# Kernel optimization log

Hardware: AMD Instinct MI355X
Metric: run time of the kernel (lower is better)

## Reference

```python
import jax, jax.numpy as jnp
import numpy as np

INPUT_SIZE = 24
OUTPUT_SIZE = 24
HIDDEN = 40
BATCH = 4096
SEQ = 256


def setup_inputs() -> dict:
    key = jax.random.key(0)
    ks = jax.random.split(key, 7)
    s = 1.0 / np.sqrt(HIDDEN)  # torch RNN/Linear default uniform bound
    x = jax.random.normal(ks[0], (BATCH, SEQ, INPUT_SIZE), dtype=jnp.float32)
    W_ih = jax.random.uniform(ks[1], (3 * HIDDEN, INPUT_SIZE), jnp.float32, -s, s)
    W_hh = jax.random.uniform(ks[2], (3 * HIDDEN, HIDDEN), jnp.float32, -s, s)
    b_ih = jax.random.uniform(ks[3], (3 * HIDDEN,), jnp.float32, -s, s)
    b_hh = jax.random.uniform(ks[4], (3 * HIDDEN,), jnp.float32, -s, s)
    W_fc = jax.random.uniform(ks[5], (OUTPUT_SIZE, HIDDEN), jnp.float32, -s, s)
    b_fc = jax.random.uniform(ks[6], (OUTPUT_SIZE,), jnp.float32, -s, s)
    return {"x": x, "W_ih": W_ih, "W_hh": W_hh, "b_ih": b_ih,
            "b_hh": b_hh, "W_fc": W_fc, "b_fc": b_fc}


def _gru_forward(x, W_ih, W_hh, b_ih, b_hh):
    # PyTorch GRU gate order: reset, update, new. Precompute input projections.
    B, T, _ = x.shape
    H = W_hh.shape[1]
    xg = jnp.einsum('bti,gi->btg', x, W_ih) + b_ih  # [B, T, 3H]

    def step(h, xg_t):
        hg = h @ W_hh.T + b_hh                      # [B, 3H]
        xr, xz, xn = jnp.split(xg_t, 3, axis=-1)
        hr, hz, hn = jnp.split(hg, 3, axis=-1)
        r = jax.nn.sigmoid(xr + hr)
        z = jax.nn.sigmoid(xz + hz)
        n = jnp.tanh(xn + r * hn)
        h_new = (1.0 - z) * n + z * h
        return h_new, h_new

    h0 = jnp.zeros((B, H), dtype=x.dtype)
    hT, outs = jax.lax.scan(step, h0, jnp.swapaxes(xg, 0, 1))  # outs: [T, B, H]
    return jnp.swapaxes(outs, 0, 1), hT                        # [B, T, H], [B, H]


def reference(x, W_ih, W_hh, b_ih, b_hh, W_fc, b_fc):
    seq_out, hT = _gru_forward(x, W_ih, W_hh, b_ih, b_hh)
    H = W_hh.shape[1]
    out = seq_out.reshape(-1, H)                   # [B*T, H]
    out = jax.nn.sigmoid(out @ W_fc.T + b_fc)      # [B*T, output_size]
    hidden = hT[None]                              # [n_layers=1, B, H]
    return out, hidden
```

## Files before the change

### kernel.cpp

```cpp
#include <hip/hip_runtime.h>
#include <math.h>

typedef __attribute__((ext_vector_type(8))) short short8;
typedef __attribute__((ext_vector_type(4))) float f32x4;

namespace {
constexpr int BATCH = 4096;
constexpr int SEQT  = 256;
constexpr int INSZ  = 24;
constexpr int H     = 40;
constexpr int NOUT  = 24;
constexpr int R     = 16;
constexpr int NT    = 256;

__device__ __forceinline__ unsigned short f2bf(float f) {
  unsigned int u = __float_as_uint(f);
  return (unsigned short)((u + 0x7FFFu + ((u >> 16) & 1u)) >> 16);
}
__device__ __forceinline__ unsigned short cvt_bf16(float f) {
  float r;
  asm("v_cvt_pk_bf16_f32 %0, %1, %2" : "=v"(r) : "v"(f), "v"(f));
  return (unsigned short)__float_as_uint(r);
}
__device__ __forceinline__ unsigned int cvt_pk2(float lo, float hi) {
  float r;
  asm("v_cvt_pk_bf16_f32 %0, %1, %2" : "=v"(r) : "v"(lo), "v"(hi));
  return __float_as_uint(r);
}
__device__ __forceinline__ float4 ld4(const float* p) {
  return *reinterpret_cast<const float4*>(p);
}
__device__ __forceinline__ float sigm(float v) {
  return __builtin_amdgcn_rcpf(1.0f + __builtin_amdgcn_exp2f(v * -1.442695041f));
}
__device__ __forceinline__ float tanh_fast(float v) {
  return fmaf(2.0f,
              __builtin_amdgcn_rcpf(1.0f + __builtin_amdgcn_exp2f(v * -2.885390082f)),
              -1.0f);
}
}

#define BAR()                                              \
  asm volatile("s_waitcnt lgkmcnt(0)" ::: "memory");       \
  __builtin_amdgcn_s_barrier();                            \
  __builtin_amdgcn_sched_barrier(0);

#define MFMA16(A, Bf, C) __builtin_amdgcn_mfma_f32_16x16x32_bf16((A), (Bf), (C), 0, 0, 0)

__global__ __launch_bounds__(NT) void gru_ilp2(
    const float* __restrict__ x, const float* __restrict__ Wih,
    const float* __restrict__ Whh, const float* __restrict__ bih,
    const float* __restrict__ bhh, const float* __restrict__ Wfc,
    const float* __restrict__ bfc, float* __restrict__ out,
    float* __restrict__ hid) {
  __shared__ __align__(16) unsigned short Abuf[4 * 1024];

  const int tid = threadIdx.x;
  const int l   = tid & 63;
  const int w   = tid >> 6;
  const int lm  = l & 15;
  const int lq  = l >> 4;
  const int gb0 = blockIdx.x * R;

  reinterpret_cast<uint4*>(Abuf)[tid]       = make_uint4(0, 0, 0, 0);
  reinterpret_cast<uint4*>(Abuf)[tid + 256] = make_uint4(0, 0, 0, 0);

  const int aBase0 = ((lm * 64 + lq * 8)      ^ ((lm & 7) << 3));
  const int aBase1 = ((lm * 64 + lq * 8 + 32) ^ ((lm & 7) << 3));

  short8 B[4][2];
  float bias[4] = {0, 0, 0, 0};
  float hold[2][2] = {{0, 0}, {0, 0}};
  int aw[2] = {0, 0};
  int u = 0;
  bool gvalid = false;
  if (w < 3) {
    u = w * 16 + lm;
    gvalid = (u < H);
#pragma unroll
    for (int z = 0; z < 4; ++z) {
#pragma unroll
      for (int kt = 0; kt < 2; ++kt) {
        short8 b;
#pragma unroll
        for (int j = 0; j < 8; ++j) {
          const int k = kt * 32 + lq * 8 + j;
          float v = 0.0f;
          if (gvalid) {
            if (z == 0)      v = (k < 24) ? Wih[u * 24 + k]          : Whh[u * 40 + (k - 24)];
            else if (z == 1) v = (k < 24) ? Wih[(40 + u) * 24 + k]   : Whh[(40 + u) * 40 + (k - 24)];
            else if (z == 2) v = (k < 24) ? Wih[(80 + u) * 24 + k]   : 0.0f;
            else             v = (k < 24) ? 0.0f                     : Whh[(80 + u) * 40 + (k - 24)];
          }
          b[j] = (short)f2bf(v);
        }
        B[z][kt] = b;
      }
    }
    if (gvalid) {
      bias[0] = bih[u] + bhh[u];
      bias[1] = bih[40 + u] + bhh[40 + u];
      bias[2] = bih[80 + u];
      bias[3] = bhh[80 + u];
    }
#pragma unroll
    for (int i = 0; i < 2; ++i) {
      const int arow = lq * 4 + i;
      aw[i] = ((arow * 64 + 24 + u) ^ ((arow & 7) << 3));
    }
  }

  short8 F[2][2];
  float biasF[2] = {0, 0};
  float* orow[2][2] = {{nullptr, nullptr}, {nullptr, nullptr}};
  const float* xpg[2] = {nullptr, nullptr};
  int xw0 = 0;
  bool xv = false;
  float4 aQ1 = make_float4(0,0,0,0), aQ2 = make_float4(0,0,0,0);
  float4 aQ3 = make_float4(0,0,0,0), aQ0 = make_float4(0,0,0,0);
  float4 bQ1 = make_float4(0,0,0,0), bQ2 = make_float4(0,0,0,0);
  float4 bQ3 = make_float4(0,0,0,0), bQ0 = make_float4(0,0,0,0);
  if (w == 3) {
#pragma unroll
    for (int f = 0; f < 2; ++f) {
      const int o = f * 16 + lm;
#pragma unroll
      for (int kt = 0; kt < 2; ++kt) {
        short8 b;
#pragma unroll
        for (int j = 0; j < 8; ++j) {
          const int k = kt * 32 + lq * 8 + j;
          const float v = (o < NOUT && k >= 24) ? Wfc[o * H + (k - 24)] : 0.0f;
          b[j] = (short)f2bf(v);
        }
        F[f][kt] = b;
      }
      biasF[f] = (o < NOUT) ? bfc[o] : 0.0f;
    }
#pragma unroll
    for (int g = 0; g < 2; ++g)
#pragma unroll
      for (int i = 0; i < 2; ++i)
        orow[g][i] = out + ((size_t)(gb0 + g * 8 + lq * 2 + i) * SEQT) * NOUT;

    xv = (l < 48);
    const int xr = l / 6, xc = (l - xr * 6) * 4;
    const int ar_ = ((xr >> 1) << 2) + (xr & 1);
    if (xv) {
      xpg[0] = x + ((size_t)(gb0 + xr) * SEQT) * INSZ + xc;
      xpg[1] = x + ((size_t)(gb0 + 8 + xr) * SEQT) * INSZ + xc;
    }
    xw0 = ((ar_ * 64 + xc) ^ ((ar_ & 7) << 3));
  }

  const f32x4 kZero = {0.0f, 0.0f, 0.0f, 0.0f};

  __syncthreads();

  if (w == 3 && xv) {
    const float4 v0 = ld4(xpg[0]);
    *reinterpret_cast<uint2*>(&Abuf[xw0]) =
        make_uint2(cvt_pk2(v0.x, v0.y), cvt_pk2(v0.z, v0.w));
    const float4 v1 = ld4(xpg[1]);
    *reinterpret_cast<uint2*>(&Abuf[2048 + xw0]) =
        make_uint2(cvt_pk2(v1.x, v1.y), cvt_pk2(v1.z, v1.w));
    aQ1 = ld4(xpg[0] + 1 * INSZ);  bQ1 = ld4(xpg[1] + 1 * INSZ);
    aQ2 = ld4(xpg[0] + 2 * INSZ);  bQ2 = ld4(xpg[1] + 2 * INSZ);
    aQ3 = ld4(xpg[0] + 3 * INSZ);  bQ3 = ld4(xpg[1] + 3 * INSZ);
    aQ0 = ld4(xpg[0] + 4 * INSZ);  bQ0 = ld4(xpg[1] + 4 * INSZ);
  }
  __syncthreads();

#define GATE2(BO, NBO)                                                          \
  if (w < 3) {                                                                  \
    const short8 A00 = *reinterpret_cast<const short8*>(&Abuf[(BO) + aBase0]);  \
    const short8 A01 = *reinterpret_cast<const short8*>(&Abuf[(BO) + aBase1]);  \
    const short8 A10 = *reinterpret_cast<const short8*>(&Abuf[2048 + (BO) + aBase0]); \
    const short8 A11 = *reinterpret_cast<const short8*>(&Abuf[2048 + (BO) + aBase1]); \
    f32x4 ar0 = MFMA16(A00, B[0][0], kZero);                                    \
    f32x4 az0 = MFMA16(A00, B[1][0], kZero);                                    \
    f32x4 ax0 = MFMA16(A00, B[2][0], kZero);                                    \
    f32x4 ah0 = MFMA16(A00, B[3][0], kZero);                                    \
    f32x4 ar1 = MFMA16(A10, B[0][0], kZero);                                    \
    f32x4 az1 = MFMA16(A10, B[1][0], kZero);                                    \
    f32x4 ax1 = MFMA16(A10, B[2][0], kZero);                                    \
    f32x4 ah1 = MFMA16(A10, B[3][0], kZero);                                    \
    ar0 = MFMA16(A01, B[0][1], ar0);                                            \
    az0 = MFMA16(A01, B[1][1], az0);                                            \
    ah0 = MFMA16(A01, B[3][1], ah0);                                            \
    ar1 = MFMA16(A11, B[0][1], ar1);                                            \
    az1 = MFMA16(A11, B[1][1], az1);                                            \
    ah1 = MFMA16(A11, B[3][1], ah1);                                            \
    _Pragma("unroll")                                                           \
    for (int i = 0; i < 2; ++i) {                                               \
      const float rr = sigm(ar0[i] + bias[0]);                                  \
      const float zz = sigm(az0[i] + bias[1]);                                  \
      const float nn = tanh_fast(fmaf(rr, ah0[i] + bias[3], ax0[i] + bias[2])); \
      const float h  = fmaf(zz, hold[0][i] - nn, nn);                           \
      hold[0][i] = h;                                                           \
      if (gvalid) Abuf[(NBO) + aw[i]] = cvt_bf16(h);                            \
    }                                                                           \
    _Pragma("unroll")                                                           \
    for (int i = 0; i < 2; ++i) {                                               \
      const float rr = sigm(ar1[i] + bias[0]);                                  \
      const float zz = sigm(az1[i] + bias[1]);                                  \
      const float nn = tanh_fast(fmaf(rr, ah1[i] + bias[3], ax1[i] + bias[2])); \
      const float h  = fmaf(zz, hold[1][i] - nn, nn);                           \
      hold[1][i] = h;                                                           \
      if (gvalid) Abuf[2048 + (NBO) + aw[i]] = cvt_bf16(h);                     \
    }                                                                           \
  }

#define XSTAGE2(T, TBO, XSa, XSb)                                               \
  if (xv) {                                                                     \
    if ((T) < SEQT) {                                                           \
      *reinterpret_cast<uint2*>(&Abuf[(TBO) + xw0]) =                           \
          make_uint2(cvt_pk2(XSa.x, XSa.y), cvt_pk2(XSa.z, XSa.w));             \
      *reinterpret_cast<uint2*>(&Abuf[2048 + (TBO) + xw0]) =                    \
          make_uint2(cvt_pk2(XSb.x, XSb.y), cvt_pk2(XSb.z, XSb.w));             \
    }                                                                           \
    if ((T) + 4 < SEQT) {                                                       \
      XSa = ld4(xpg[0] + (size_t)((T) + 4) * INSZ);                             \
      XSb = ld4(xpg[1] + (size_t)((T) + 4) * INSZ);                             \
    }                                                                           \
  }

#define FC2(T, BO)                                                              \
  {                                                                             \
    const short8 hA00 = *reinterpret_cast<const short8*>(&Abuf[(BO) + aBase0]); \
    const short8 hA01 = *reinterpret_cast<const short8*>(&Abuf[(BO) + aBase1]); \
    const short8 hA10 = *reinterpret_cast<const short8*>(&Abuf[2048 + (BO) + aBase0]); \
    const short8 hA11 = *reinterpret_cast<const short8*>(&Abuf[2048 + (BO) + aBase1]); \
    f32x4 f00 = MFMA16(hA00, F[0][0], kZero);                                   \
    f32x4 f01 = MFMA16(hA00, F[1][0], kZero);                                   \
    f32x4 f10 = MFMA16(hA10, F[0][0], kZero);                                   \
    f32x4 f11 = MFMA16(hA10, F[1][0], kZero);                                   \
    f00 = MFMA16(hA01, F[0][1], f00);                                           \
    f01 = MFMA16(hA01, F[1][1], f01);                                           \
    f10 = MFMA16(hA11, F[0][1], f10);                                           \
    f11 = MFMA16(hA11, F[1][1], f11);                                           \
    _Pragma("unroll")                                                           \
    for (int i = 0; i < 2; ++i) {                                               \
      orow[0][i][(size_t)(T) * NOUT + lm] = sigm(f00[i] + biasF[0]);            \
      orow[1][i][(size_t)(T) * NOUT + lm] = sigm(f10[i] + biasF[0]);            \
      if (lm < 8) {                                                             \
        orow[0][i][(size_t)(T) * NOUT + 16 + lm] = sigm(f01[i] + biasF[1]);     \
        orow[1][i][(size_t)(T) * NOUT + 16 + lm] = sigm(f11[i] + biasF[1]);     \
      }                                                                         \
    }                                                                           \
  }

  for (int tt = 0; tt < SEQT; tt += 4) {
    GATE2(0, 1024)
    if (w == 3) {
      XSTAGE2(tt + 1, 1024, aQ1, bQ1)
      if (tt > 0) FC2(tt - 1, 0)
    }
    BAR()
    GATE2(1024, 0)
    if (w == 3) {
      XSTAGE2(tt + 2, 0, aQ2, bQ2)
      FC2(tt, 1024)
    }
    BAR()
    GATE2(0, 1024)
    if (w == 3) {
      XSTAGE2(tt + 3, 1024, aQ3, bQ3)
      FC2(tt + 1, 0)
    }
    BAR()
    GATE2(1024, 0)
    if (w == 3) {
      XSTAGE2(tt + 4, 0, aQ0, bQ0)
      FC2(tt + 2, 1024)
    }
    BAR()
  }
  if (w == 3) FC2(SEQT - 1, 0)

  if (w < 3 && gvalid) {
#pragma unroll
    for (int g = 0; g < 2; ++g)
#pragma unroll
      for (int i = 0; i < 2; ++i)
        hid[(size_t)(gb0 + g * 8 + lq * 2 + i) * H + u] = hold[g][i];
  }
}

extern "C" void kernel_launch(void* const* d_in, const int* in_sizes, int n_in,
                              void* d_out, int out_size, void* d_ws, size_t ws_size,
                              hipStream_t stream) {
  const float* x   = (const float*)d_in[0];
  const float* Wih = (const float*)d_in[1];
  const float* Whh = (const float*)d_in[2];
  const float* bih = (const float*)d_in[3];
  const float* bhh = (const float*)d_in[4];
  const float* Wfc = (const float*)d_in[5];
  const float* bfc = (const float*)d_in[6];
  float* out = (float*)d_out;
  float* hid = out + (size_t)BATCH * SEQT * NOUT;

  dim3 grid(BATCH / R);
  dim3 block(NT);
  hipLaunchKernelGGL(gru_ilp2, grid, block, 0, stream,
                     x, Wih, Whh, bih, bhh, Wfc, bfc, out, hid);
}
```

Before: 138.0 us.

## Halve batch rows per block to double grid size for more occupancy

```diff
diff --git a/kernel.cpp b/kernel.cpp
--- a/kernel.cpp
+++ b/kernel.cpp
@@ -10,7 +10,7 @@
 constexpr int INSZ  = 24;
 constexpr int H     = 40;
 constexpr int NOUT  = 24;
-constexpr int R     = 16;
+constexpr int R     = 8;
 constexpr int NT    = 256;
 
 __device__ __forceinline__ unsigned short f2bf(float f) {
@@ -47,7 +47,7 @@
 
 #define MFMA16(A, Bf, C) __builtin_amdgcn_mfma_f32_16x16x32_bf16((A), (Bf), (C), 0, 0, 0)
 
-__global__ __launch_bounds__(NT) void gru_ilp2(
+__global__ __launch_bounds__(NT) void gru_q4(
     const float* __restrict__ x, const float* __restrict__ Wih,
     const float* __restrict__ Whh, const float* __restrict__ bih,
     const float* __restrict__ bhh, const float* __restrict__ Wfc,
@@ -70,8 +70,8 @@
 
   short8 B[4][2];
   float bias[4] = {0, 0, 0, 0};
-  float hold[2][2] = {{0, 0}, {0, 0}};
-  int aw[2] = {0, 0};
+  float hold[2] = {0, 0};
+  int aw0 = 0;
   int u = 0;
   bool gvalid = false;
   if (w < 3) {
@@ -103,23 +103,20 @@
       bias[2] = bih[80 + u];
       bias[3] = bhh[80 + u];
     }
-#pragma unroll
-    for (int i = 0; i < 2; ++i) {
-      const int arow = lq * 4 + i;
-      aw[i] = ((arow * 64 + 24 + u) ^ ((arow & 7) << 3));
+    {
+      const int arow = lq * 4;
+      aw0 = ((arow * 64 + 24 + u) ^ ((arow & 7) << 3));
     }
   }
 
   short8 F[2][2];
   float biasF[2] = {0, 0};
-  float* orow[2][2] = {{nullptr, nullptr}, {nullptr, nullptr}};
-  const float* xpg[2] = {nullptr, nullptr};
-  int xw0 = 0;
+  float* orow[2] = {nullptr, nullptr};
+  const float* xp0 = nullptr;
+  int xwBase = 0;
   bool xv = false;
-  float4 aQ1 = make_float4(0,0,0,0), aQ2 = make_float4(0,0,0,0);
-  float4 aQ3 = make_float4(0,0,0,0), aQ0 = make_float4(0,0,0,0);
-  float4 bQ1 = make_float4(0,0,0,0), bQ2 = make_float4(0,0,0,0);
-  float4 bQ3 = make_float4(0,0,0,0), bQ0 = make_float4(0,0,0,0);
+  float4 xQ1 = make_float4(0,0,0,0), xQ2 = make_float4(0,0,0,0);
+  float4 xQ3 = make_float4(0,0,0,0), xQ0 = make_float4(0,0,0,0);
   if (w == 3) {
 #pragma unroll
     for (int f = 0; f < 2; ++f) {
@@ -139,18 +136,15 @@
     }
 #pragma unroll
     for (int g = 0; g < 2; ++g)
-#pragma unroll
-      for (int i = 0; i < 2; ++i)
-        orow[g][i] = out + ((size_t)(gb0 + g * 8 + lq * 2 + i) * SEQT) * NOUT;
+      orow[g] = out + ((size_t)(gb0 + g * 4 + lq) * SEQT) * NOUT;
 
     xv = (l < 48);
-    const int xr = l / 6, xc = (l - xr * 6) * 4;
-    const int ar_ = ((xr >> 1) << 2) + (xr & 1);
-    if (xv) {
-      xpg[0] = x + ((size_t)(gb0 + xr) * SEQT) * INSZ + xc;
-      xpg[1] = x + ((size_t)(gb0 + 8 + xr) * SEQT) * INSZ + xc;
-    }
-    xw0 = ((ar_ * 64 + xc) ^ ((ar_ & 7) << 3));
+    const int g  = l / 24;
+    const int m  = l - g * 24;
+    const int xr = m / 6, xc = (m - xr * 6) * 4;
+    const int ar_ = xr << 2;
+    if (xv) xp0 = x + ((size_t)(gb0 + g * 4 + xr) * SEQT) * INSZ + xc;
+    xwBase = (g << 11) + ((ar_ * 64 + xc) ^ ((ar_ & 7) << 3));
   }
 
   const f32x4 kZero = {0.0f, 0.0f, 0.0f, 0.0f};
@@ -158,16 +152,13 @@
   __syncthreads();
 
   if (w == 3 && xv) {
-    const float4 v0 = ld4(xpg[0]);
-    *reinterpret_cast<uint2*>(&Abuf[xw0]) =
+    const float4 v0 = ld4(xp0);
+    *reinterpret_cast<uint2*>(&Abuf[xwBase]) =
         make_uint2(cvt_pk2(v0.x, v0.y), cvt_pk2(v0.z, v0.w));
-    const float4 v1 = ld4(xpg[1]);
-    *reinterpret_cast<uint2*>(&Abuf[2048 + xw0]) =
-        make_uint2(cvt_pk2(v1.x, v1.y), cvt_pk2(v1.z, v1.w));
-    aQ1 = ld4(xpg[0] + 1 * INSZ);  bQ1 = ld4(xpg[1] + 1 * INSZ);
-    aQ2 = ld4(xpg[0] + 2 * INSZ);  bQ2 = ld4(xpg[1] + 2 * INSZ);
-    aQ3 = ld4(xpg[0] + 3 * INSZ);  bQ3 = ld4(xpg[1] + 3 * INSZ);
-    aQ0 = ld4(xpg[0] + 4 * INSZ);  bQ0 = ld4(xpg[1] + 4 * INSZ);
+    xQ1 = ld4(xp0 + 1 * INSZ);
+    xQ2 = ld4(xp0 + 2 * INSZ);
+    xQ3 = ld4(xp0 + 3 * INSZ);
+    xQ0 = ld4(xp0 + 4 * INSZ);
   }
   __syncthreads();
 
@@ -191,38 +182,31 @@
     ar1 = MFMA16(A11, B[0][1], ar1);                                            \
     az1 = MFMA16(A11, B[1][1], az1);                                            \
     ah1 = MFMA16(A11, B[3][1], ah1);                                            \
-    _Pragma("unroll")                                                           \
-    for (int i = 0; i < 2; ++i) {                                               \
-      const float rr = sigm(ar0[i] + bias[0]);                                  \
-      const float zz = sigm(az0[i] + bias[1]);                                  \
-      const float nn = tanh_fast(fmaf(rr, ah0[i] + bias[3], ax0[i] + bias[2])); \
-      const float h  = fmaf(zz, hold[0][i] - nn, nn);                           \
-      hold[0][i] = h;                                                           \
-      if (gvalid) Abuf[(NBO) + aw[i]] = cvt_bf16(h);                            \
-    }                                                                           \
-    _Pragma("unroll")                                                           \
-    for (int i = 0; i < 2; ++i) {                                               \
-      const float rr = sigm(ar1[i] + bias[0]);                                  \
-      const float zz = sigm(az1[i] + bias[1]);                                  \
-      const float nn = tanh_fast(fmaf(rr, ah1[i] + bias[3], ax1[i] + bias[2])); \
-      const float h  = fmaf(zz, hold[1][i] - nn, nn);                           \
-      hold[1][i] = h;                                                           \
-      if (gvalid) Abuf[2048 + (NBO) + aw[i]] = cvt_bf16(h);                     \
-    }                                                                           \
-  }
-
-#define XSTAGE2(T, TBO, XSa, XSb)                                               \
+    {                                                                           \
+      const float rr = sigm(ar0[0] + bias[0]);                                  \
+      const float zz = sigm(az0[0] + bias[1]);                                  \
+      const float nn = tanh_fast(fmaf(rr, ah0[0] + bias[3], ax0[0] + bias[2])); \
+      const float h  = fmaf(zz, hold[0] - nn, nn);                              \
+      hold[0] = h;                                                              \
+      if (gvalid) Abuf[(NBO) + aw0] = cvt_bf16(h);                              \
+    }                                                                           \
+    {                                                                           \
+      const float rr = sigm(ar1[0] + bias[0]);                                  \
+      const float zz = sigm(az1[0] + bias[1]);                                  \
+      const float nn = tanh_fast(fmaf(rr, ah1[0] + bias[3], ax1[0] + bias[2])); \
+      const float h  = fmaf(zz, hold[1] - nn, nn);                              \
+      hold[1] = h;                                                              \
+      if (gvalid) Abuf[2048 + (NBO) + aw0] = cvt_bf16(h);                       \
+    }                                                                           \
+  }
+
+#define XSTAGE(T, TBO, XS)                                                      \
   if (xv) {                                                                     \
     if ((T) < SEQT) {                                                           \
-      *reinterpret_cast<uint2*>(&Abuf[(TBO) + xw0]) =                           \
-          make_uint2(cvt_pk2(XSa.x, XSa.y), cvt_pk2(XSa.z, XSa.w));             \
-      *reinterpret_cast<uint2*>(&Abuf[2048 + (TBO) + xw0]) =                    \
-          make_uint2(cvt_pk2(XSb.x, XSb.y), cvt_pk2(XSb.z, XSb.w));             \
-    }                                                                           \
-    if ((T) + 4 < SEQT) {                                                       \
-      XSa = ld4(xpg[0] + (size_t)((T) + 4) * INSZ);                             \
-      XSb = ld4(xpg[1] + (size_t)((T) + 4) * INSZ);                             \
-    }                                                                           \
+      *reinterpret_cast<uint2*>(&Abuf[(TBO) + xwBase]) =                        \
+          make_uint2(cvt_pk2(XS.x, XS.y), cvt_pk2(XS.z, XS.w));                 \
+    }                                                                           \
+    if ((T) + 4 < SEQT) XS = ld4(xp0 + (size_t)((T) + 4) * INSZ);               \
   }
 
 #define FC2(T, BO)                                                              \
@@ -239,39 +223,36 @@
     f01 = MFMA16(hA01, F[1][1], f01);                                           \
     f10 = MFMA16(hA11, F[0][1], f10);                                           \
     f11 = MFMA16(hA11, F[1][1], f11);                                           \
-    _Pragma("unroll")                                                           \
-    for (int i = 0; i < 2; ++i) {                                               \
-      orow[0][i][(size_t)(T) * NOUT + lm] = sigm(f00[i] + biasF[0]);            \
-      orow[1][i][(size_t)(T) * NOUT + lm] = sigm(f10[i] + biasF[0]);            \
-      if (lm < 8) {                                                             \
-        orow[0][i][(size_t)(T) * NOUT + 16 + lm] = sigm(f01[i] + biasF[1]);     \
-        orow[1][i][(size_t)(T) * NOUT + 16 + lm] = sigm(f11[i] + biasF[1]);     \
-      }                                                                         \
+    orow[0][(size_t)(T) * NOUT + lm] = sigm(f00[0] + biasF[0]);                 \
+    orow[1][(size_t)(T) * NOUT + lm] = sigm(f10[0] + biasF[0]);                 \
+    if (lm < 8) {                                                               \
+      orow[0][(size_t)(T) * NOUT + 16 + lm] = sigm(f01[0] + biasF[1]);          \
+      orow[1][(size_t)(T) * NOUT + 16 + lm] = sigm(f11[0] + biasF[1]);          \
     }                                                                           \
   }
 
   for (int tt = 0; tt < SEQT; tt += 4) {
     GATE2(0, 1024)
     if (w == 3) {
-      XSTAGE2(tt + 1, 1024, aQ1, bQ1)
+      XSTAGE(tt + 1, 1024, xQ1)
       if (tt > 0) FC2(tt - 1, 0)
     }
     BAR()
     GATE2(1024, 0)
     if (w == 3) {
-      XSTAGE2(tt + 2, 0, aQ2, bQ2)
+      XSTAGE(tt + 2, 0, xQ2)
       FC2(tt, 1024)
     }
     BAR()
     GATE2(0, 1024)
     if (w == 3) {
-      XSTAGE2(tt + 3, 1024, aQ3, bQ3)
+      XSTAGE(tt + 3, 1024, xQ3)
       FC2(tt + 1, 0)
     }
     BAR()
     GATE2(1024, 0)
     if (w == 3) {
-      XSTAGE2(tt + 4, 0, aQ0, bQ0)
+      XSTAGE(tt + 4, 0, xQ0)
       FC2(tt + 2, 1024)
     }
     BAR()
@@ -281,9 +262,7 @@
   if (w < 3 && gvalid) {
 #pragma unroll
     for (int g = 0; g < 2; ++g)
-#pragma unroll
-      for (int i = 0; i < 2; ++i)
-        hid[(size_t)(gb0 + g * 8 + lq * 2 + i) * H + u] = hold[g][i];
+      hid[(size_t)(gb0 + g * 4 + lq) * H + u] = hold[g];
   }
 }
 
@@ -302,6 +281,6 @@
 
   dim3 grid(BATCH / R);
   dim3 block(NT);
-  hipLaunchKernelGGL(gru_ilp2, grid, block, 0, stream,
+  hipLaunchKernelGGL(gru_q4, grid, block, 0, stream,
                      x, Wih, Whh, bih, bhh, Wfc, bfc, out, hid);
 }
```

New measurement: 135.4 us. Within noise of the previous version (-1.9%).
